# Optimization experiments

Hardware: AMD Instinct MI355X
Metric: run time of the kernel (lower is better)

## Reference

```python
import jax, jax.numpy as jnp
import numpy as np

N_NODES = 500000
N_EDGES = 5000000


def _sage_conv(x, edge_index, Wl, bl, Wr):
    # PyG SAGEConv (aggr='mean', root_weight=True):
    #   out = lin_l(mean_{j in N(i)} x_j) + lin_r(x_i)
    # edge_index[0] = source, edge_index[1] = target
    src, dst = edge_index[0], edge_index[1]
    n = x.shape[0]
    msg = x[src]  # [E, F] gather
    agg = jax.ops.segment_sum(msg, dst, num_segments=n)  # [N, F]
    deg = jax.ops.segment_sum(jnp.ones((src.shape[0],), x.dtype), dst, num_segments=n)
    agg = agg / jnp.maximum(deg, 1.0)[:, None]  # mean aggregation
    return agg @ Wl.T + bl + x @ Wr.T


def setup_inputs() -> dict:
    key = jax.random.key(0)
    k1, k2, k3, k4, k5, k6 = jax.random.split(key, 6)
    x = jax.random.normal(k1, (N_NODES, 2), dtype=jnp.float32)
    edge_index = jax.random.randint(k2, (2, N_EDGES), 0, N_NODES, dtype=jnp.int64)
    # conv1: SAGEConv(2, 16); conv2: SAGEConv(16, 1)
    s1 = 1.0 / np.sqrt(2.0)
    s2 = 1.0 / np.sqrt(16.0)
    W1l = jax.random.uniform(k3, (16, 2), jnp.float32, -s1, s1)
    W1r = jax.random.uniform(k4, (16, 2), jnp.float32, -s1, s1)
    b1 = jnp.zeros((16,), jnp.float32)
    W2l = jax.random.uniform(k5, (1, 16), jnp.float32, -s2, s2)
    W2r = jax.random.uniform(k6, (1, 16), jnp.float32, -s2, s2)
    b2 = jnp.zeros((1,), jnp.float32)
    return {"x": x, "edge_index": edge_index,
            "W1l": W1l, "b1": b1, "W1r": W1r,
            "W2l": W2l, "b2": b2, "W2r": W2r}


def reference(x, edge_index, W1l, b1, W1r, W2l, b2, W2r):
    h = jax.nn.relu(_sage_conv(x, edge_index, W1l, b1, W1r))  # [N, 16]
    h = _sage_conv(h, edge_index, W2l, b2, W2r)               # [N, 1]
    return jax.nn.sigmoid(h).squeeze(-1)                      # [N]
```

## Files before the change

kernel.cpp:

```cpp
#include <hip/hip_runtime.h>


static constexpr int ABLOCK = 512;
static constexpr int PBLOCK = 1024;
static constexpr int KITER  = 5;
static constexpr int CHUNK  = PBLOCK * 4 * KITER;
static constexpr int BUCKET_BITS = 10;
static constexpr int BUCKET_NODES = 1 << BUCKET_BITS;
static constexpr int MAXNB = 512;
static constexpr int NGRP = 8;
static constexpr int GCAP = 2048;
static constexpr int CSTRIDE = 16;

static constexpr float S1 = 2048.0f;
static constexpr float IS1 = 1.0f / 2048.0f;
static constexpr long long B1 = 8LL * 2048LL;
static constexpr float S2 = 256.0f;
static constexpr float IS2 = 1.0f / 256.0f;

__global__ __launch_bounds__(256) void k_pre(
    const float* __restrict__ x, unsigned* __restrict__ qx,
    unsigned* __restrict__ cursor, int N, int NBG)
{
    int i = blockIdx.x * 256 + threadIdx.x;
    if (i < NBG) cursor[(size_t)i * CSTRIDE] = (unsigned)i * (unsigned)GCAP;
    if (i >= N) return;
    float2 xv = *reinterpret_cast<const float2*>(x + 2 * (size_t)i);
    float f0 = fminf(fmaxf((xv.x + 8.0f) * S1, 0.0f), 65535.0f);
    float f1 = fminf(fmaxf((xv.y + 8.0f) * S1, 0.0f), 65535.0f);
    unsigned q0 = (unsigned)__float2int_rn(f0);
    unsigned q1 = (unsigned)__float2int_rn(f1);
    qx[i] = (q0 << 16) | q1;
}

__global__ __launch_bounds__(PBLOCK) void k_part(
    const int* __restrict__ src, const int* __restrict__ dst,
    unsigned* __restrict__ cursor, unsigned* __restrict__ entries,
    int E, int NB)
{
    __shared__ unsigned sorted[CHUNK];
    __shared__ unsigned hist[MAXNB];
    __shared__ unsigned loc[MAXNB];
    __shared__ unsigned base[MAXNB];
    __shared__ unsigned wsum[8];
    const int tid = threadIdx.x;
    const unsigned g = blockIdx.x & (NGRP - 1);
    const int e0 = (int)blockIdx.x * CHUNK;
    const int e1 = min(e0 + CHUNK, E);
    const int4* dst4 = reinterpret_cast<const int4*>(dst + e0);
    const int4* src4 = reinterpret_cast<const int4*>(src + e0);

    int4 dR[KITER], sR[KITER];
#pragma unroll
    for (int k = 0; k < KITER; ++k) {
        int gi = tid + k * PBLOCK;
        int e = e0 + 4 * gi;
        if (e + 3 < e1) {
            dR[k] = dst4[gi];
            sR[k] = src4[gi];
        } else {
            dR[k] = make_int4(-1, -1, -1, -1);
            sR[k] = make_int4(0, 0, 0, 0);
#pragma unroll
            for (int j = 0; j < 4; ++j) {
                if (e + j < e1) {
                    (&dR[k].x)[j] = dst[e + j];
                    (&sR[k].x)[j] = src[e + j];
                }
            }
        }
    }

    for (int b = tid; b < MAXNB; b += PBLOCK) hist[b] = 0;
    __syncthreads();

    #define HIST1(dv) { unsigned du_ = (unsigned)(dv); \
        if (du_ != 0xFFFFFFFFu) atomicAdd(&hist[du_ >> BUCKET_BITS], 1u); }
#pragma unroll
    for (int k = 0; k < KITER; ++k) {
        HIST1(dR[k].x) HIST1(dR[k].y) HIST1(dR[k].z) HIST1(dR[k].w)
    }
    #undef HIST1
    __syncthreads();

    {
        unsigned lane6 = (unsigned)tid & 63u, wv = (unsigned)tid >> 6;
        unsigned hv = (tid < NB) ? hist[tid] : 0u;
        if (tid < 512) {
            unsigned v = hv;
#pragma unroll
            for (int off = 1; off < 64; off <<= 1) {
                unsigned u = __shfl_up(v, off);
                if (lane6 >= (unsigned)off) v += u;
            }
            if (lane6 == 63) wsum[wv] = v;
            if (tid < NB) loc[tid] = v - hv;
        }
        __syncthreads();
        if (tid == 0) {
            unsigned acc = 0;
#pragma unroll
            for (int k = 0; k < 8; ++k) { unsigned t2 = wsum[k]; wsum[k] = acc; acc += t2; }
        }
        __syncthreads();
        if (tid < NB) loc[tid] += wsum[wv];
    }

    if (tid < NB) {
        int b = tid + (int)(blockIdx.x % (unsigned)NB);
        if (b >= NB) b -= NB;
        base[b] = atomicAdd(&cursor[((size_t)b * NGRP + g) * CSTRIDE], hist[b]);
    }
    __syncthreads();
    for (int b = tid; b < MAXNB; b += PBLOCK) hist[b] = 0;
    __syncthreads();

    #define SCAT1(dv, sv) { unsigned du_ = (unsigned)(dv); \
        if (du_ != 0xFFFFFFFFu) { \
            unsigned bk_ = du_ >> BUCKET_BITS; \
            unsigned r_ = atomicAdd(&hist[bk_], 1u); \
            sorted[loc[bk_] + r_] = ((unsigned)(sv) << BUCKET_BITS) | (du_ & (BUCKET_NODES - 1)); } }
#pragma unroll
    for (int k = 0; k < KITER; ++k) {
        SCAT1(dR[k].x, sR[k].x) SCAT1(dR[k].y, sR[k].y)
        SCAT1(dR[k].z, sR[k].z) SCAT1(dR[k].w, sR[k].w)
    }
    #undef SCAT1
    __syncthreads();

    const int wave = tid >> 6, lane = tid & 63;
    const int nw = PBLOCK >> 6;
    const int off = (int)(blockIdx.x % (unsigned)NB);
    for (int j = wave; j < NB; j += nw) {
        int b = j + off;
        if (b >= NB) b -= NB;
        unsigned cnt = hist[b];
        if (cnt == 0) continue;
        unsigned lo = loc[b], ba = base[b];
        unsigned lim = ((unsigned)b * NGRP + g + 1u) * (unsigned)GCAP;
        if (ba >= lim) continue;
        cnt = min(cnt, lim - ba);
        for (unsigned i = lane; i < cnt; i += 64)
            entries[ba + i] = sorted[lo + i];
    }
}

#define PK(q) ((1ULL << 56) | ((unsigned long long)((q) >> 16) << 28) \
               | (unsigned long long)((q) & 0xFFFFu))

__global__ __launch_bounds__(ABLOCK) void k_agg1(
    const unsigned* __restrict__ entries, const unsigned* __restrict__ cursor,
    const unsigned* __restrict__ qx, const float* __restrict__ x,
    const float* __restrict__ W1l, const float* __restrict__ b1,
    const float* __restrict__ W1r, const float* __restrict__ W2l,
    const float* __restrict__ W2r, const float* __restrict__ b2,
    unsigned short* __restrict__ sq, float2* __restrict__ tg,
    int N)
{
    __shared__ unsigned long long qs[BUCKET_NODES];
    int bk = blockIdx.x;
    for (int i = threadIdx.x; i < BUCKET_NODES; i += ABLOCK) qs[i] = 0ULL;
    __syncthreads();

    {
        const unsigned wv = (unsigned)threadIdx.x >> 6;
        const unsigned lane = (unsigned)threadIdx.x & 63u;
        const unsigned seg = (unsigned)bk * NGRP + wv;
        const unsigned base0 = seg * (unsigned)GCAP;
        unsigned end = min(cursor[(size_t)seg * CSTRIDE], base0 + (unsigned)GCAP);
        unsigned len = end - base0;
        unsigned t = 0;
        for (; t + 512 <= len; t += 512) {
            const uint4* p = reinterpret_cast<const uint4*>(entries + base0 + t + (lane << 3));
            uint4 a = p[0];
            uint4 b = p[1];
            unsigned g0 = qx[a.x >> BUCKET_BITS];
            unsigned g1 = qx[a.y >> BUCKET_BITS];
            unsigned g2 = qx[a.z >> BUCKET_BITS];
            unsigned g3 = qx[a.w >> BUCKET_BITS];
            unsigned g4 = qx[b.x >> BUCKET_BITS];
            unsigned g5 = qx[b.y >> BUCKET_BITS];
            unsigned g6 = qx[b.z >> BUCKET_BITS];
            unsigned g7 = qx[b.w >> BUCKET_BITS];
            atomicAdd(&qs[a.x & (BUCKET_NODES - 1)], PK(g0));
            atomicAdd(&qs[a.y & (BUCKET_NODES - 1)], PK(g1));
            atomicAdd(&qs[a.z & (BUCKET_NODES - 1)], PK(g2));
            atomicAdd(&qs[a.w & (BUCKET_NODES - 1)], PK(g3));
            atomicAdd(&qs[b.x & (BUCKET_NODES - 1)], PK(g4));
            atomicAdd(&qs[b.y & (BUCKET_NODES - 1)], PK(g5));
            atomicAdd(&qs[b.z & (BUCKET_NODES - 1)], PK(g6));
            atomicAdd(&qs[b.w & (BUCKET_NODES - 1)], PK(g7));
        }
        for (unsigned u = t + lane; u < len; u += 64) {
            unsigned en = entries[base0 + u];
            unsigned gq = qx[en >> BUCKET_BITS];
            atomicAdd(&qs[en & (BUCKET_NODES - 1)], PK(gq));
        }
    }
    __syncthreads();

    int nodebase = bk << BUCKET_BITS;
    for (int il = threadIdx.x; il < BUCKET_NODES; il += ABLOCK) {
        int i = nodebase + il;
        if (i >= N) continue;
        unsigned long long v = qs[il];
        int deg = (int)(v >> 56);
        long long q0 = (long long)((v >> 28) & 0xFFFFFFFULL);
        long long q1 = (long long)(v & 0xFFFFFFFULL);
        long long bias = (long long)deg * B1;
        float inv = 1.0f / (float)max(deg, 1);
        float m0 = (float)(q0 - bias) * IS1 * inv;
        float m1 = (float)(q1 - bias) * IS1 * inv;
        float2 xv = *reinterpret_cast<const float2*>(x + 2 * (size_t)i);
        float s = 0.0f, t0 = b2[0];
#pragma unroll
        for (int o = 0; o < 16; ++o) {
            float h = m0 * W1l[2 * o] + m1 * W1l[2 * o + 1] + b1[o]
                    + xv.x * W1r[2 * o] + xv.y * W1r[2 * o + 1];
            h = fmaxf(h, 0.0f);
            s  += h * W2l[o];
            t0 += h * W2r[o];
        }
        float fq = fminf(fmaxf((s + 128.0f) * S2, 0.0f), 65535.0f);
        sq[i] = (unsigned short)__float2int_rn(fq);
        tg[i] = make_float2(IS2 * inv, t0 - (deg > 0 ? 128.0f : 0.0f));
    }
}

__global__ __launch_bounds__(ABLOCK) void k_agg2(
    const unsigned* __restrict__ entries, const unsigned* __restrict__ cursor,
    const unsigned short* __restrict__ sq,
    const float2* __restrict__ tg,
    float* __restrict__ out, int N)
{
    __shared__ unsigned sbin[BUCKET_NODES];
    int bk = blockIdx.x;
    for (int i = threadIdx.x; i < BUCKET_NODES; i += ABLOCK) sbin[i] = 0;
    __syncthreads();

    {
        const unsigned wv = (unsigned)threadIdx.x >> 6;
        const unsigned lane = (unsigned)threadIdx.x & 63u;
        const unsigned seg = (unsigned)bk * NGRP + wv;
        const unsigned base0 = seg * (unsigned)GCAP;
        unsigned end = min(cursor[(size_t)seg * CSTRIDE], base0 + (unsigned)GCAP);
        unsigned len = end - base0;
        unsigned t = 0;
        for (; t + 512 <= len; t += 512) {
            const uint4* p = reinterpret_cast<const uint4*>(entries + base0 + t + (lane << 3));
            uint4 a = p[0];
            uint4 b = p[1];
            unsigned v0 = sq[a.x >> BUCKET_BITS];
            unsigned v1 = sq[a.y >> BUCKET_BITS];
            unsigned v2 = sq[a.z >> BUCKET_BITS];
            unsigned v3 = sq[a.w >> BUCKET_BITS];
            unsigned v4 = sq[b.x >> BUCKET_BITS];
            unsigned v5 = sq[b.y >> BUCKET_BITS];
            unsigned v6 = sq[b.z >> BUCKET_BITS];
            unsigned v7 = sq[b.w >> BUCKET_BITS];
            atomicAdd(&sbin[a.x & (BUCKET_NODES - 1)], v0);
            atomicAdd(&sbin[a.y & (BUCKET_NODES - 1)], v1);
            atomicAdd(&sbin[a.z & (BUCKET_NODES - 1)], v2);
            atomicAdd(&sbin[a.w & (BUCKET_NODES - 1)], v3);
            atomicAdd(&sbin[b.x & (BUCKET_NODES - 1)], v4);
            atomicAdd(&sbin[b.y & (BUCKET_NODES - 1)], v5);
            atomicAdd(&sbin[b.z & (BUCKET_NODES - 1)], v6);
            atomicAdd(&sbin[b.w & (BUCKET_NODES - 1)], v7);
        }
        for (unsigned u = t + lane; u < len; u += 64) {
            unsigned en = entries[base0 + u];
            atomicAdd(&sbin[en & (BUCKET_NODES - 1)], (unsigned)sq[en >> BUCKET_BITS]);
        }
    }
    __syncthreads();

    int nodebase = bk << BUCKET_BITS;
    for (int il = threadIdx.x; il < BUCKET_NODES; il += ABLOCK) {
        int i = nodebase + il;
        if (i >= N) continue;
        float2 tgv = tg[i];
        float t = (float)(int)sbin[il] * tgv.x + tgv.y;
        out[i] = 1.0f / (1.0f + expf(-t));
    }
}

__global__ __launch_bounds__(256) void k_scatter1_fb(
    const int* __restrict__ src, const int* __restrict__ dst,
    const float* __restrict__ x, float* __restrict__ agg1, float* __restrict__ deg, int E)
{
    int stride = gridDim.x * blockDim.x;
    for (int e = blockIdx.x * blockDim.x + threadIdx.x; e < E; e += stride) {
        int s = src[e], d = dst[e];
        float2 xv = *reinterpret_cast<const float2*>(x + 2 * (size_t)s);
        unsafeAtomicAdd(&agg1[2 * (size_t)d + 0], xv.x);
        unsafeAtomicAdd(&agg1[2 * (size_t)d + 1], xv.y);
        unsafeAtomicAdd(&deg[d], 1.0f);
    }
}
__global__ __launch_bounds__(256) void k_node1_fb(
    const float* __restrict__ x, const float* __restrict__ agg1, const float* __restrict__ deg,
    const float* __restrict__ W1l, const float* __restrict__ b1,
    const float* __restrict__ W1r, const float* __restrict__ W2l,
    float* __restrict__ sval, int N)
{
    int i = blockIdx.x * blockDim.x + threadIdx.x;
    if (i >= N) return;
    float inv = 1.0f / fmaxf(deg[i], 1.0f);
    float2 a = *reinterpret_cast<const float2*>(agg1 + 2 * (size_t)i);
    float m0 = a.x * inv, m1 = a.y * inv;
    float2 xv = *reinterpret_cast<const float2*>(x + 2 * (size_t)i);
    float s = 0.0f;
#pragma unroll
    for (int o = 0; o < 16; ++o) {
        float h = m0 * W1l[2 * o] + m1 * W1l[2 * o + 1] + b1[o]
                + xv.x * W1r[2 * o] + xv.y * W1r[2 * o + 1];
        s += fmaxf(h, 0.0f) * W2l[o];
    }
    sval[i] = s;
}
__global__ __launch_bounds__(256) void k_scatter2_fb(
    const int* __restrict__ src, const int* __restrict__ dst,
    const float* __restrict__ sval, float* __restrict__ agg_s, int E)
{
    int stride = gridDim.x * blockDim.x;
    for (int e = blockIdx.x * blockDim.x + threadIdx.x; e < E; e += stride)
        unsafeAtomicAdd(&agg_s[dst[e]], sval[src[e]]);
}
__global__ __launch_bounds__(256) void k_node2_fb(
    const float* __restrict__ x, const float* __restrict__ agg1, const float* __restrict__ deg,
    const float* __restrict__ agg_s,
    const float* __restrict__ W1l, const float* __restrict__ b1,
    const float* __restrict__ W1r, const float* __restrict__ W2r, const float* __restrict__ b2,
    float* __restrict__ out, int N)
{
    int i = blockIdx.x * blockDim.x + threadIdx.x;
    if (i >= N) return;
    float inv = 1.0f / fmaxf(deg[i], 1.0f);
    float2 a = *reinterpret_cast<const float2*>(agg1 + 2 * (size_t)i);
    float m0 = a.x * inv, m1 = a.y * inv;
    float2 xv = *reinterpret_cast<const float2*>(x + 2 * (size_t)i);
    float t = agg_s[i] * inv + b2[0];
#pragma unroll
    for (int o = 0; o < 16; ++o) {
        float h = m0 * W1l[2 * o] + m1 * W1l[2 * o + 1] + b1[o]
                + xv.x * W1r[2 * o] + xv.y * W1r[2 * o + 1];
        t += fmaxf(h, 0.0f) * W2r[o];
    }
    out[i] = 1.0f / (1.0f + expf(-t));
}

extern "C" void kernel_launch(void* const* d_in, const int* in_sizes, int n_in,
                              void* d_out, int out_size, void* d_ws, size_t ws_size,
                              hipStream_t stream) {
    const float* x   = (const float*)d_in[0];
    const int*   ei  = (const int*)d_in[1];
    const float* W1l = (const float*)d_in[2];
    const float* b1  = (const float*)d_in[3];
    const float* W1r = (const float*)d_in[4];
    const float* W2l = (const float*)d_in[5];
    const float* b2  = (const float*)d_in[6];
    const float* W2r = (const float*)d_in[7];

    const int N = in_sizes[0] / 2;
    const int E = in_sizes[1] / 2;
    const int* src = ei;
    const int* dst = ei + (size_t)E;
    float* out = (float*)d_out;

    const int NB = (N + BUCKET_NODES - 1) >> BUCKET_BITS;
    const int NBG = NB * NGRP;
    const int pblocks = (E + CHUNK - 1) / CHUNK;

    size_t needed = (size_t)MAXNB * NGRP * CSTRIDE * 4
                  + (size_t)NBG * GCAP * 4
                  + ((size_t)N * 2 + 3) / 4 * 4
                  + (size_t)N * 8 + (size_t)N * 4 + 256;
    if (NB <= MAXNB && NB <= PBLOCK && ws_size >= needed) {
        unsigned* cursor   = (unsigned*)d_ws;
        unsigned* entries  = cursor + (size_t)MAXNB * NGRP * CSTRIDE;
        unsigned short* sq = (unsigned short*)(entries + (size_t)NBG * GCAP);
        float2*   tg       = (float2*)((char*)sq + (((size_t)N * 2 + 7) & ~7ull));
        unsigned* qx       = (unsigned*)(tg + N);

        k_pre<<<(N + 255) / 256, 256, 0, stream>>>(x, qx, cursor, N, NBG);
        k_part<<<pblocks, PBLOCK, 0, stream>>>(src, dst, cursor, entries, E, NB);
        k_agg1<<<NB, ABLOCK, 0, stream>>>(entries, cursor, qx, x, W1l, b1, W1r,
                                          W2l, W2r, b2, sq, tg, N);
        k_agg2<<<NB, ABLOCK, 0, stream>>>(entries, cursor, sq, tg, out, N);
    } else {
        float* agg1  = (float*)d_ws;
        float* deg   = agg1 + 2 * (size_t)N;
        float* agg_s = deg + (size_t)N;
        float* sval  = agg_s + (size_t)N;
        hipMemsetAsync(d_ws, 0, 4 * (size_t)N * sizeof(float), stream);
        const int eblocks = 2048, nblocks = (N + 255) / 256;
        k_scatter1_fb<<<eblocks, 256, 0, stream>>>(src, dst, x, agg1, deg, E);
        k_node1_fb<<<nblocks, 256, 0, stream>>>(x, agg1, deg, W1l, b1, W1r, W2l, sval, N);
        k_scatter2_fb<<<eblocks, 256, 0, stream>>>(src, dst, sval, agg_s, E);
        k_node2_fb<<<nblocks, 256, 0, stream>>>(x, agg1, deg, agg_s, W1l, b1, W1r, W2r, b2, out, N);
    }
}
```

Baseline: 91.74 us.

## Use single per-bucket segment and per-wave-group shared histograms in partition

Replaces the eight per-bucket global cursor groups (selected by block index) with one contiguous segment per bucket of capacity 16384, so aggregation blocks read one contiguous range with all threads instead of one wave per group segment. In the partition kernel, the shared-memory histogram is split into eight replicas indexed by thread group to reduce LDS atomic contention, with per-replica offsets computed before scattering. The cost is more global atomic contention on a single cursor per bucket and extra shared memory and prefix work per block.

After: 90.21 us. Within noise of the previous version (-1.7%).

```diff
diff --git a/kernel.cpp b/kernel.cpp
--- a/kernel.cpp
+++ b/kernel.cpp
@@ -8,8 +8,8 @@
 static constexpr int BUCKET_BITS = 10;
 static constexpr int BUCKET_NODES = 1 << BUCKET_BITS;
 static constexpr int MAXNB = 512;
-static constexpr int NGRP = 8;
-static constexpr int GCAP = 2048;
+static constexpr int NR = 8;
+static constexpr int CAP = 16384;
 static constexpr int CSTRIDE = 16;
 
 static constexpr float S1 = 2048.0f;
@@ -20,10 +20,10 @@
 
 __global__ __launch_bounds__(256) void k_pre(
     const float* __restrict__ x, unsigned* __restrict__ qx,
-    unsigned* __restrict__ cursor, int N, int NBG)
+    unsigned* __restrict__ cursor, int N, int NB)
 {
     int i = blockIdx.x * 256 + threadIdx.x;
-    if (i < NBG) cursor[(size_t)i * CSTRIDE] = (unsigned)i * (unsigned)GCAP;
+    if (i < NB) cursor[(size_t)i * CSTRIDE] = (unsigned)i * (unsigned)CAP;
     if (i >= N) return;
     float2 xv = *reinterpret_cast<const float2*>(x + 2 * (size_t)i);
     float f0 = fminf(fmaxf((xv.x + 8.0f) * S1, 0.0f), 65535.0f);
@@ -39,12 +39,14 @@
     int E, int NB)
 {
     __shared__ unsigned sorted[CHUNK];
+    __shared__ unsigned histR[NR][MAXNB + 1];
+    __shared__ unsigned offR[NR][MAXNB + 1];
     __shared__ unsigned hist[MAXNB];
     __shared__ unsigned loc[MAXNB];
     __shared__ unsigned base[MAXNB];
     __shared__ unsigned wsum[8];
     const int tid = threadIdx.x;
-    const unsigned g = blockIdx.x & (NGRP - 1);
+    const int g = tid >> 7;
     const int e0 = (int)blockIdx.x * CHUNK;
     const int e1 = min(e0 + CHUNK, E);
     const int4* dst4 = reinterpret_cast<const int4*>(dst + e0);
@@ -71,11 +73,12 @@
         }
     }
 
-    for (int b = tid; b < MAXNB; b += PBLOCK) hist[b] = 0;
+    for (int i = tid; i < NR * (MAXNB + 1); i += PBLOCK)
+        (&histR[0][0])[i] = 0;
     __syncthreads();
 
     #define HIST1(dv) { unsigned du_ = (unsigned)(dv); \
-        if (du_ != 0xFFFFFFFFu) atomicAdd(&hist[du_ >> BUCKET_BITS], 1u); }
+        if (du_ != 0xFFFFFFFFu) atomicAdd(&histR[g][du_ >> BUCKET_BITS], 1u); }
 #pragma unroll
     for (int k = 0; k < KITER; ++k) {
         HIST1(dR[k].x) HIST1(dR[k].y) HIST1(dR[k].z) HIST1(dR[k].w)
@@ -83,10 +86,18 @@
     #undef HIST1
     __syncthreads();
 
+    if (tid < NB) {
+        unsigned acc = 0;
+#pragma unroll
+        for (int k = 0; k < NR; ++k) { offR[k][tid] = acc; acc += histR[k][tid]; }
+        hist[tid] = acc;
+    }
+    __syncthreads();
+
     {
         unsigned lane6 = (unsigned)tid & 63u, wv = (unsigned)tid >> 6;
-        unsigned hv = (tid < NB) ? hist[tid] : 0u;
         if (tid < 512) {
+            unsigned hv = (tid < NB) ? hist[tid] : 0u;
             unsigned v = hv;
 #pragma unroll
             for (int off = 1; off < 64; off <<= 1) {
@@ -109,17 +120,19 @@
     if (tid < NB) {
         int b = tid + (int)(blockIdx.x % (unsigned)NB);
         if (b >= NB) b -= NB;
-        base[b] = atomicAdd(&cursor[((size_t)b * NGRP + g) * CSTRIDE], hist[b]);
-    }
-    __syncthreads();
-    for (int b = tid; b < MAXNB; b += PBLOCK) hist[b] = 0;
+        base[b] = atomicAdd(&cursor[(size_t)b * CSTRIDE], hist[b]);
+    }
+    __syncthreads();
+    for (int i = tid; i < NR * (MAXNB + 1); i += PBLOCK)
+        (&histR[0][0])[i] = 0;
     __syncthreads();
 
     #define SCAT1(dv, sv) { unsigned du_ = (unsigned)(dv); \
         if (du_ != 0xFFFFFFFFu) { \
             unsigned bk_ = du_ >> BUCKET_BITS; \
-            unsigned r_ = atomicAdd(&hist[bk_], 1u); \
-            sorted[loc[bk_] + r_] = ((unsigned)(sv) << BUCKET_BITS) | (du_ & (BUCKET_NODES - 1)); } }
+            unsigned r_ = atomicAdd(&histR[g][bk_], 1u); \
+            sorted[loc[bk_] + offR[g][bk_] + r_] = \
+                ((unsigned)(sv) << BUCKET_BITS) | (du_ & (BUCKET_NODES - 1)); } }
 #pragma unroll
     for (int k = 0; k < KITER; ++k) {
         SCAT1(dR[k].x, sR[k].x) SCAT1(dR[k].y, sR[k].y)
@@ -137,7 +150,7 @@
         unsigned cnt = hist[b];
         if (cnt == 0) continue;
         unsigned lo = loc[b], ba = base[b];
-        unsigned lim = ((unsigned)b * NGRP + g + 1u) * (unsigned)GCAP;
+        unsigned lim = (unsigned)(b + 1) * (unsigned)CAP;
         if (ba >= lim) continue;
         cnt = min(cnt, lim - ba);
         for (unsigned i = lane; i < cnt; i += 64)
@@ -162,40 +175,36 @@
     for (int i = threadIdx.x; i < BUCKET_NODES; i += ABLOCK) qs[i] = 0ULL;
     __syncthreads();
 
-    {
-        const unsigned wv = (unsigned)threadIdx.x >> 6;
-        const unsigned lane = (unsigned)threadIdx.x & 63u;
-        const unsigned seg = (unsigned)bk * NGRP + wv;
-        const unsigned base0 = seg * (unsigned)GCAP;
-        unsigned end = min(cursor[(size_t)seg * CSTRIDE], base0 + (unsigned)GCAP);
-        unsigned len = end - base0;
-        unsigned t = 0;
-        for (; t + 512 <= len; t += 512) {
-            const uint4* p = reinterpret_cast<const uint4*>(entries + base0 + t + (lane << 3));
-            uint4 a = p[0];
-            uint4 b = p[1];
-            unsigned g0 = qx[a.x >> BUCKET_BITS];
-            unsigned g1 = qx[a.y >> BUCKET_BITS];
-            unsigned g2 = qx[a.z >> BUCKET_BITS];
-            unsigned g3 = qx[a.w >> BUCKET_BITS];
-            unsigned g4 = qx[b.x >> BUCKET_BITS];
-            unsigned g5 = qx[b.y >> BUCKET_BITS];
-            unsigned g6 = qx[b.z >> BUCKET_BITS];
-            unsigned g7 = qx[b.w >> BUCKET_BITS];
-            atomicAdd(&qs[a.x & (BUCKET_NODES - 1)], PK(g0));
-            atomicAdd(&qs[a.y & (BUCKET_NODES - 1)], PK(g1));
-            atomicAdd(&qs[a.z & (BUCKET_NODES - 1)], PK(g2));
-            atomicAdd(&qs[a.w & (BUCKET_NODES - 1)], PK(g3));
-            atomicAdd(&qs[b.x & (BUCKET_NODES - 1)], PK(g4));
-            atomicAdd(&qs[b.y & (BUCKET_NODES - 1)], PK(g5));
-            atomicAdd(&qs[b.z & (BUCKET_NODES - 1)], PK(g6));
-            atomicAdd(&qs[b.w & (BUCKET_NODES - 1)], PK(g7));
-        }
-        for (unsigned u = t + lane; u < len; u += 64) {
-            unsigned en = entries[base0 + u];
-            unsigned gq = qx[en >> BUCKET_BITS];
-            atomicAdd(&qs[en & (BUCKET_NODES - 1)], PK(gq));
-        }
+    unsigned start = (unsigned)bk * (unsigned)CAP;
+    unsigned end = min(cursor[(size_t)bk * CSTRIDE], start + (unsigned)CAP);
+    unsigned n = end - start;
+    unsigned n8 = n >> 3;
+    const uint4* e4 = reinterpret_cast<const uint4*>(entries + start);
+
+    for (unsigned t = threadIdx.x; t < n8; t += ABLOCK) {
+        uint4 a = e4[2 * t];
+        uint4 b = e4[2 * t + 1];
+        unsigned g0 = qx[a.x >> BUCKET_BITS];
+        unsigned g1 = qx[a.y >> BUCKET_BITS];
+        unsigned g2 = qx[a.z >> BUCKET_BITS];
+        unsigned g3 = qx[a.w >> BUCKET_BITS];
+        unsigned g4 = qx[b.x >> BUCKET_BITS];
+        unsigned g5 = qx[b.y >> BUCKET_BITS];
+        unsigned g6 = qx[b.z >> BUCKET_BITS];
+        unsigned g7 = qx[b.w >> BUCKET_BITS];
+        atomicAdd(&qs[a.x & (BUCKET_NODES - 1)], PK(g0));
+        atomicAdd(&qs[a.y & (BUCKET_NODES - 1)], PK(g1));
+        atomicAdd(&qs[a.z & (BUCKET_NODES - 1)], PK(g2));
+        atomicAdd(&qs[a.w & (BUCKET_NODES - 1)], PK(g3));
+        atomicAdd(&qs[b.x & (BUCKET_NODES - 1)], PK(g4));
+        atomicAdd(&qs[b.y & (BUCKET_NODES - 1)], PK(g5));
+        atomicAdd(&qs[b.z & (BUCKET_NODES - 1)], PK(g6));
+        atomicAdd(&qs[b.w & (BUCKET_NODES - 1)], PK(g7));
+    }
+    for (unsigned t = start + (n8 << 3) + threadIdx.x; t < end; t += ABLOCK) {
+        unsigned en = entries[t];
+        unsigned gq = qx[en >> BUCKET_BITS];
+        atomicAdd(&qs[en & (BUCKET_NODES - 1)], PK(gq));
     }
     __syncthreads();
 
@@ -238,39 +247,35 @@
     for (int i = threadIdx.x; i < BUCKET_NODES; i += ABLOCK) sbin[i] = 0;
     __syncthreads();
 
-    {
-        const unsigned wv = (unsigned)threadIdx.x >> 6;
-        const unsigned lane = (unsigned)threadIdx.x & 63u;
-        const unsigned seg = (unsigned)bk * NGRP + wv;
-        const unsigned base0 = seg * (unsigned)GCAP;
-        unsigned end = min(cursor[(size_t)seg * CSTRIDE], base0 + (unsigned)GCAP);
-        unsigned len = end - base0;
-        unsigned t = 0;
-        for (; t + 512 <= len; t += 512) {
-            const uint4* p = reinterpret_cast<const uint4*>(entries + base0 + t + (lane << 3));
-            uint4 a = p[0];
-            uint4 b = p[1];
-            unsigned v0 = sq[a.x >> BUCKET_BITS];
-            unsigned v1 = sq[a.y >> BUCKET_BITS];
-            unsigned v2 = sq[a.z >> BUCKET_BITS];
-            unsigned v3 = sq[a.w >> BUCKET_BITS];
-            unsigned v4 = sq[b.x >> BUCKET_BITS];
-            unsigned v5 = sq[b.y >> BUCKET_BITS];
-            unsigned v6 = sq[b.z >> BUCKET_BITS];
-            unsigned v7 = sq[b.w >> BUCKET_BITS];
-            atomicAdd(&sbin[a.x & (BUCKET_NODES - 1)], v0);
-            atomicAdd(&sbin[a.y & (BUCKET_NODES - 1)], v1);
-            atomicAdd(&sbin[a.z & (BUCKET_NODES - 1)], v2);
-            atomicAdd(&sbin[a.w & (BUCKET_NODES - 1)], v3);
-            atomicAdd(&sbin[b.x & (BUCKET_NODES - 1)], v4);
-            atomicAdd(&sbin[b.y & (BUCKET_NODES - 1)], v5);
-            atomicAdd(&sbin[b.z & (BUCKET_NODES - 1)], v6);
-            atomicAdd(&sbin[b.w & (BUCKET_NODES - 1)], v7);
-        }
-        for (unsigned u = t + lane; u < len; u += 64) {
-            unsigned en = entries[base0 + u];
-            atomicAdd(&sbin[en & (BUCKET_NODES - 1)], (unsigned)sq[en >> BUCKET_BITS]);
-        }
+    unsigned start = (unsigned)bk * (unsigned)CAP;
+    unsigned end = min(cursor[(size_t)bk * CSTRIDE], start + (unsigned)CAP);
+    unsigned n = end - start;
+    unsigned n8 = n >> 3;
+    const uint4* e4 = reinterpret_cast<const uint4*>(entries + start);
+
+    for (unsigned t = threadIdx.x; t < n8; t += ABLOCK) {
+        uint4 a = e4[2 * t];
+        uint4 b = e4[2 * t + 1];
+        unsigned v0 = sq[a.x >> BUCKET_BITS];
+        unsigned v1 = sq[a.y >> BUCKET_BITS];
+        unsigned v2 = sq[a.z >> BUCKET_BITS];
+        unsigned v3 = sq[a.w >> BUCKET_BITS];
+        unsigned v4 = sq[b.x >> BUCKET_BITS];
+        unsigned v5 = sq[b.y >> BUCKET_BITS];
+        unsigned v6 = sq[b.z >> BUCKET_BITS];
+        unsigned v7 = sq[b.w >> BUCKET_BITS];
+        atomicAdd(&sbin[a.x & (BUCKET_NODES - 1)], v0);
+        atomicAdd(&sbin[a.y & (BUCKET_NODES - 1)], v1);
+        atomicAdd(&sbin[a.z & (BUCKET_NODES - 1)], v2);
+        atomicAdd(&sbin[a.w & (BUCKET_NODES - 1)], v3);
+        atomicAdd(&sbin[b.x & (BUCKET_NODES - 1)], v4);
+        atomicAdd(&sbin[b.y & (BUCKET_NODES - 1)], v5);
+        atomicAdd(&sbin[b.z & (BUCKET_NODES - 1)], v6);
+        atomicAdd(&sbin[b.w & (BUCKET_NODES - 1)], v7);
+    }
+    for (unsigned t = start + (n8 << 3) + threadIdx.x; t < end; t += ABLOCK) {
+        unsigned en = entries[t];
+        atomicAdd(&sbin[en & (BUCKET_NODES - 1)], (unsigned)sq[en >> BUCKET_BITS]);
     }
     __syncthreads();
 
@@ -368,21 +373,20 @@
     float* out = (float*)d_out;
 
     const int NB = (N + BUCKET_NODES - 1) >> BUCKET_BITS;
-    const int NBG = NB * NGRP;
     const int pblocks = (E + CHUNK - 1) / CHUNK;
 
-    size_t needed = (size_t)MAXNB * NGRP * CSTRIDE * 4
-                  + (size_t)NBG * GCAP * 4
-                  + ((size_t)N * 2 + 3) / 4 * 4
+    size_t needed = (size_t)MAXNB * CSTRIDE * 4
+                  + (size_t)NB * CAP * 4
+                  + (((size_t)N * 2 + 7) & ~7ull)
                   + (size_t)N * 8 + (size_t)N * 4 + 256;
     if (NB <= MAXNB && NB <= PBLOCK && ws_size >= needed) {
         unsigned* cursor   = (unsigned*)d_ws;
-        unsigned* entries  = cursor + (size_t)MAXNB * NGRP * CSTRIDE;
-        unsigned short* sq = (unsigned short*)(entries + (size_t)NBG * GCAP);
+        unsigned* entries  = cursor + (size_t)MAXNB * CSTRIDE;
+        unsigned short* sq = (unsigned short*)(entries + (size_t)NB * CAP);
         float2*   tg       = (float2*)((char*)sq + (((size_t)N * 2 + 7) & ~7ull));
         unsigned* qx       = (unsigned*)(tg + N);
 
-        k_pre<<<(N + 255) / 256, 256, 0, stream>>>(x, qx, cursor, N, NBG);
+        k_pre<<<(N + 255) / 256, 256, 0, stream>>>(x, qx, cursor, N, NB);
         k_part<<<pblocks, PBLOCK, 0, stream>>>(src, dst, cursor, entries, E, NB);
         k_agg1<<<NB, ABLOCK, 0, stream>>>(entries, cursor, qx, x, W1l, b1, W1r,
                                           W2l, W2r, b2, sq, tg, N);
```
